# Optimization experiments

Measured on AMD Instinct MI355X. Metric: run time of the kernel, lower is better.

Reference implementation:

```python
import jax, jax.numpy as jnp
import numpy as np

LN_EPS = 1e-5


def _layernorm(x, g, b):
    m = jnp.mean(x, axis=-1, keepdims=True)
    v = jnp.mean((x - m) ** 2, axis=-1, keepdims=True)
    return (x - m) * jax.lax.rsqrt(v + LN_EPS) * g + b


def _gcn_conv(x, row, col, ew, W, b):
    # linear projection
    x = x @ W + b  # [N, out]
    n = x.shape[0]
    # weighted degree per source node (index_add over row)
    deg = jax.ops.segment_sum(ew, row, num_segments=n)  # [N]
    safe = jnp.where(deg > 0, deg, 1.0)
    dis = jnp.where(deg > 0, jax.lax.rsqrt(safe), 0.0)  # deg^-0.5, inf -> 0
    norm = dis[row] * ew * dis[col]  # [E]
    # gather-scale-scatter aggregation
    return jax.ops.segment_sum(norm[:, None] * x[col], row, num_segments=n)


def setup_inputs() -> dict:
    key = jax.random.key(0)
    ks = jax.random.split(key, 8)
    N, E, D_IN, D_H, D_OUT = 50000, 800000, 384, 256, 128
    x = jax.random.normal(ks[0], (N, D_IN), dtype=jnp.float32)
    edge_index = jax.random.randint(ks[1], (2, E), 0, N, dtype=jnp.int64)
    edge_weight = jax.random.uniform(ks[2], (E,), dtype=jnp.float32)
    W1 = jax.random.normal(ks[3], (D_IN, D_H), dtype=jnp.float32) * 0.02
    b1 = jnp.zeros((D_H,), dtype=jnp.float32)
    W2 = jax.random.normal(ks[4], (D_H, D_OUT), dtype=jnp.float32) * 0.02
    b2 = jnp.zeros((D_OUT,), dtype=jnp.float32)
    g1 = jnp.ones((D_H,), dtype=jnp.float32)
    be1 = jnp.zeros((D_H,), dtype=jnp.float32)
    g2 = jnp.ones((D_OUT,), dtype=jnp.float32)
    be2 = jnp.zeros((D_OUT,), dtype=jnp.float32)
    return {"x": x, "edge_index": edge_index, "edge_weight": edge_weight,
            "W1": W1, "b1": b1, "W2": W2, "b2": b2,
            "g1": g1, "be1": be1, "g2": g2, "be2": be2}


def reference(x, edge_index, edge_weight, W1, b1, W2, b2, g1, be1, g2, be2):
    row, col = edge_index[0], edge_index[1]
    h = _gcn_conv(x, row, col, edge_weight, W1, b1)
    h = _layernorm(h, g1, be1)
    h = jax.nn.relu(h)
    # dropout is identity in eval mode
    h = _gcn_conv(h, row, col, edge_weight, W2, b2)
    h = _layernorm(h, g2, be2)
    return h
```

## Files before the change

kernel.cpp:

```cpp
#include <hip/hip_runtime.h>


constexpr float LN_EPS = 1e-5f;
constexpr int   SLOTS  = 64;

typedef __attribute__((ext_vector_type(8))) short short8;
typedef __attribute__((ext_vector_type(4))) float f32x4;
typedef __attribute__((ext_vector_type(2))) float f32x2;

static __device__ __forceinline__ unsigned short f2bf(float f) {
    unsigned u = __float_as_uint(f);
    u += 0x7FFFu + ((u >> 16) & 1u);
    return (unsigned short)(u >> 16);
}
static __device__ __forceinline__ short8 f2bf8(float4 a, float4 b) {
    short8 r;
    r[0] = (short)f2bf(a.x); r[1] = (short)f2bf(a.y);
    r[2] = (short)f2bf(a.z); r[3] = (short)f2bf(a.w);
    r[4] = (short)f2bf(b.x); r[5] = (short)f2bf(b.y);
    r[6] = (short)f2bf(b.z); r[7] = (short)f2bf(b.w);
    return r;
}

#if defined(__has_builtin)
#if __has_builtin(__builtin_amdgcn_global_load_lds)
#define HAS_GLL 1
#endif
#endif

#ifdef HAS_GLL
static __device__ __forceinline__ void gll16(const void* g, void* l) {
    __builtin_amdgcn_global_load_lds(
        (__attribute__((address_space(1))) void*)g,
        (__attribute__((address_space(3))) void*)l, 16, 0, 0);
}
#endif

static __device__ __forceinline__ int swz(int r) {
    return (r & 3) ^ ((r >> 2) & 3);
}

__global__ __launch_bounds__(256) void k_hist(
    const int* __restrict__ row, const int* __restrict__ col,
    const float* __restrict__ ew, int* __restrict__ cnt,
    int2* __restrict__ edges, int E)
{
    int e = blockIdx.x * 256 + threadIdx.x;
    if (e >= E) return;
    int r = row[e];
    int o = atomicAdd(cnt + r, 1);
    if (o < SLOTS)
        edges[(size_t)r * SLOTS + o] = make_int2(col[e], __float_as_int(ew[e]));
}

__global__ __launch_bounds__(256) void k_dis(
    const int* __restrict__ cnt, const int2* __restrict__ edges,
    float* __restrict__ dis, int n)
{
    const int gw   = (blockIdx.x * 256 + threadIdx.x) >> 6;
    const int lane = threadIdx.x & 63;
    if (gw >= n) return;
    int c = cnt[gw]; if (c > SLOTS) c = SLOTS;
    float v = 0.0f;
    if (lane < c) v = __int_as_float(edges[(size_t)gw * SLOTS + lane].y);
    #pragma unroll
    for (int off = 32; off; off >>= 1) v += __shfl_xor(v, off);
    if (lane == 0) dis[gw] = v > 0.0f ? rsqrtf(v) : 0.0f;
}

__global__ __launch_bounds__(256) void k_prep(
    const float* __restrict__ W1, const float* __restrict__ W2,
    const float* __restrict__ x,
    unsigned short* __restrict__ W1P, unsigned short* __restrict__ W2P,
    unsigned short* __restrict__ xb, int nwin)
{
    constexpr int K1 = 384, N1 = 256, K2 = 256, N2 = 128;
    constexpr int WTB = (K1 * N1 + K2 * N2) / 256;
    if (blockIdx.x < WTB) {
        int o = blockIdx.x * 256 + threadIdx.x;
        if (o < K1 * N1) {
            int cc = o & 31, n = (o >> 5) % N1, p = o / (N1 * 32);
            int c = cc >> 3, j = cc & 7;
            int k = p * 32 + (((c ^ swz(n & 15)) & 3) << 3) + j;
            W1P[o] = f2bf(W1[(size_t)k * N1 + n]);
        } else {
            int o2 = o - K1 * N1;
            int cc = o2 & 31, n = (o2 >> 5) % N2, p = o2 / (N2 * 32);
            int c = cc >> 3, j = cc & 7;
            int k = p * 32 + (((c ^ swz(n & 15)) & 3) << 3) + j;
            W2P[o2] = f2bf(W2[(size_t)k * N2 + n]);
        }
    } else {
        int w = (blockIdx.x - WTB) * 256 + threadIdx.x;
        if (w >= nwin) return;
        int row = w / 12, win = w - row * 12;
        int s = swz(row & 15);
        const float* src = x + (size_t)row * 384 + win * 32;
        unsigned short* dst = xb + (size_t)row * 384 + win * 32;
        #pragma unroll
        for (int c = 0; c < 4; ++c) {
            int cs = c ^ s;
            float4 a = *(const float4*)(src + cs * 8);
            float4 b = *(const float4*)(src + cs * 8 + 4);
            *(short8*)(dst + c * 8) = f2bf8(a, b);
        }
    }
}

template<int NFULL, int K>
__global__ __launch_bounds__(256, 4) void k_gemm_mfma(
    const unsigned short* __restrict__ A, const unsigned short* __restrict__ BP,
    const float* __restrict__ bias, unsigned short* __restrict__ C, int M)
{
    constexpr int BM = 64, BN = 128, BK = 32;
    constexpr int MR = 4, NF = 2;
    constexpr int AB = BM * BK * 2;
    constexpr int BB = BN * BK * 2;
    constexpr int TB = AB + BB;

    __shared__ char smem[2 * TB];

    const int t    = threadIdx.x;
    const int lane = t & 63;
    const int wid  = t >> 6;
    const int row0 = blockIdx.x * BM;
    const int col0 = blockIdx.y * BN;
    const int fr   = lane & 15;
    const int fq   = lane >> 4;
    const int nbw  = wid * 32;
    const int nt   = K / BK;

    const int cOff = ((fq ^ swz(fr)) & 3) << 3;

    f32x4 acc[MR][NF] = {};

    auto srcA = [&](int slot, int k0) -> const void* {
        int ra = slot >> 2, ca = slot & 3;
        int gr = row0 + ra; if (gr >= M) gr = M - 1;
        return (const void*)(A + (size_t)gr * K + k0 + ca * 8);
    };
    auto srcB = [&](int slot, int st) -> const void* {
        int rb = slot >> 2, cb = slot & 3;
        return (const void*)(BP + ((size_t)st * NFULL + col0 + rb) * 32 + cb * 8);
    };

    auto compute = [&](char* buf) {
        const unsigned short* As = (const unsigned short*)buf;
        const unsigned short* Bs = (const unsigned short*)(buf + AB);
        short8 af[MR], bfr[NF];
        #pragma unroll
        for (int i = 0; i < MR; ++i)
            af[i] = *(const short8*)(As + (i * 16 + fr) * 32 + cOff);
        #pragma unroll
        for (int j = 0; j < NF; ++j)
            bfr[j] = *(const short8*)(Bs + (nbw + j * 16 + fr) * 32 + cOff);
        #pragma unroll
        for (int i = 0; i < MR; ++i)
            #pragma unroll
            for (int j = 0; j < NF; ++j)
                acc[i][j] = __builtin_amdgcn_mfma_f32_16x16x32_bf16(
                    af[i], bfr[j], acc[i][j], 0, 0, 0);
    };

#ifdef HAS_GLL
    auto stage = [&](int buf, int st) {
        char* As = smem + buf * TB;
        char* Bs = As + AB;
        gll16(srcA(t, st * BK), As + t * 16);
        gll16(srcB(t, st), Bs + t * 16);
        gll16(srcB(256 + t, st), Bs + (256 + t) * 16);
    };

    stage(0, 0);
    __syncthreads();
    int cur = 0;
    for (int st = 0; st < nt; ++st) {
        if (st + 1 < nt) stage(cur ^ 1, st + 1);
        compute(smem + cur * TB);
        __syncthreads();
        cur ^= 1;
    }
#else
    for (int st = 0; st < nt; ++st) {
        int4 ar = *(const int4*)srcA(t, st * BK);
        int4 b0 = *(const int4*)srcB(t, st);
        int4 b1 = *(const int4*)srcB(256 + t, st);
        __syncthreads();
        *(int4*)(smem + t * 16) = ar;
        *(int4*)(smem + AB + t * 16) = b0;
        *(int4*)(smem + AB + (256 + t) * 16) = b1;
        __syncthreads();
        compute(smem);
    }
#endif

    #pragma unroll
    for (int i = 0; i < MR; ++i) {
        #pragma unroll
        for (int j = 0; j < NF; ++j) {
            const int c = col0 + nbw + j * 16 + fr;
            const float bvv = bias[c];
            #pragma unroll
            for (int r = 0; r < 4; ++r) {
                const int rr = row0 + i * 16 + fq * 4 + r;
                if (rr < M)
                    C[(size_t)rr * NFULL + c] = f2bf(acc[i][j][r] + bvv);
            }
        }
    }
}

template<int D, bool RELU, bool OUTBF, bool SWZ>
__global__ __launch_bounds__(256) void k_agg_ln(
    const unsigned short* __restrict__ feat, const int* __restrict__ cnt,
    const int2* __restrict__ edges, const float* __restrict__ dis,
    const float* __restrict__ g, const float* __restrict__ b,
    void* __restrict__ outv, int n)
{
    constexpr int EV  = 16;
    constexpr int LPR = D / EV;
    constexpr int EPI = 64 / LPR;
    const int gw   = (blockIdx.x * 256 + threadIdx.x) >> 6;
    const int lane = threadIdx.x & 63;
    if (gw >= n) return;

    const int sub = lane / LPR;
    const int el  = (lane % LPR) * EV;

    int j1 = cnt[gw]; if (j1 > SLOTS) j1 = SLOTS;
    const int2* eb = edges + (size_t)gw * SLOTS;
    const float disr = dis[gw];

    f32x2 acc[8] = {};

    int2 e0 = (sub < j1)       ? eb[sub]       : make_int2(0, 0);
    int2 e1 = (EPI + sub < j1) ? eb[EPI + sub] : make_int2(0, 0);
    float dc0 = dis[e0.x];
    uint4 u0, u1;
    {
        const unsigned short* p = feat + (size_t)e0.x * D + el;
        u0 = *(const uint4*)p;
        u1 = *(const uint4*)(p + 8);
    }

    for (int j = 0; j < j1; j += EPI) {
        int2 e2 = (j + 2 * EPI + sub < j1) ? eb[j + 2 * EPI + sub]
                                           : make_int2(0, 0);
        float dc1 = dis[e1.x];
        const unsigned short* p = feat + (size_t)e1.x * D + el;
        uint4 v0 = *(const uint4*)p;
        uint4 v1 = *(const uint4*)(p + 8);

        const float wv = __int_as_float(e0.y) * dc0;
        const unsigned a[8] = {u0.x, u0.y, u0.z, u0.w, u1.x, u1.y, u1.z, u1.w};
        #pragma unroll
        for (int i = 0; i < 8; ++i) {
            f32x2 h;
            h.x = __uint_as_float(a[i] << 16);
            h.y = __uint_as_float(a[i] & 0xffff0000u);
            acc[i] += h * wv;
        }
        u0 = v0; u1 = v1; e0 = e1; e1 = e2; dc0 = dc1;
    }

    #pragma unroll
    for (int off = LPR; off < 64; off <<= 1)
        #pragma unroll
        for (int i = 0; i < 8; ++i) {
            acc[i].x += __shfl_xor(acc[i].x, off);
            acc[i].y += __shfl_xor(acc[i].y, off);
        }

    #pragma unroll
    for (int i = 0; i < 8; ++i) acc[i] *= disr;

    float s = 0.0f;
    #pragma unroll
    for (int i = 0; i < 8; ++i) s += acc[i].x + acc[i].y;
    #pragma unroll
    for (int off = 32; off; off >>= 1) s += __shfl_xor(s, off);
    const float m = s * (1.0f / (EPI * D));

    float q = 0.0f;
    #pragma unroll
    for (int i = 0; i < 8; ++i) {
        float dx = acc[i].x - m, dy = acc[i].y - m;
        q += dx * dx + dy * dy;
    }
    #pragma unroll
    for (int off = 32; off; off >>= 1) q += __shfl_xor(q, off);
    const float r = rsqrtf(q * (1.0f / (EPI * D)) + LN_EPS);

    if (lane < LPR) {
        float o[16];
        #pragma unroll
        for (int i = 0; i < 4; ++i) {
            float4 gv = *(const float4*)(g + el + i * 4);
            float4 bv = *(const float4*)(b + el + i * 4);
            const float vals[4] = {acc[2 * i].x, acc[2 * i].y,
                                   acc[2 * i + 1].x, acc[2 * i + 1].y};
            const float gg[4] = {gv.x, gv.y, gv.z, gv.w};
            const float bb[4] = {bv.x, bv.y, bv.z, bv.w};
            #pragma unroll
            for (int k2 = 0; k2 < 4; ++k2) {
                float tv = (vals[k2] - m) * r * gg[k2] + bb[k2];
                if constexpr (RELU) tv = fmaxf(tv, 0.0f);
                o[i * 4 + k2] = tv;
            }
        }
        if constexpr (OUTBF) {
            short8 lo, hi;
            #pragma unroll
            for (int i = 0; i < 8; ++i) {
                lo[i] = (short)f2bf(o[i]);
                hi[i] = (short)f2bf(o[8 + i]);
            }
            unsigned short* ob = (unsigned short*)outv + (size_t)gw * D;
            const int w0 = el & ~31;
            const int c0 = (el >> 3) & 3;
            const int sA = SWZ ? swz(gw & 15) : 0;
            *(short8*)(ob + w0 + (((c0 ^ sA) & 3) << 3))       = lo;
            *(short8*)(ob + w0 + ((((c0 + 1) ^ sA) & 3) << 3)) = hi;
        } else {
            float* op = (float*)outv + (size_t)gw * D + el;
            *(float4*)(op)      = make_float4(o[0],  o[1],  o[2],  o[3]);
            *(float4*)(op + 4)  = make_float4(o[4],  o[5],  o[6],  o[7]);
            *(float4*)(op + 8)  = make_float4(o[8],  o[9],  o[10], o[11]);
            *(float4*)(op + 12) = make_float4(o[12], o[13], o[14], o[15]);
        }
    }
}

extern "C" void kernel_launch(void* const* d_in, const int* in_sizes, int n_in,
                              void* d_out, int out_size, void* d_ws, size_t ws_size,
                              hipStream_t stream)
{
    (void)n_in; (void)out_size; (void)ws_size;

    constexpr int DIN = 384, DH = 256, DOUT = 128;

    const float* x   = (const float*)d_in[0];
    const int*   ei  = (const int*)  d_in[1];
    const float* ew  = (const float*)d_in[2];
    const float* W1  = (const float*)d_in[3];
    const float* b1  = (const float*)d_in[4];
    const float* W2  = (const float*)d_in[5];
    const float* b2  = (const float*)d_in[6];
    const float* g1  = (const float*)d_in[7];
    const float* be1 = (const float*)d_in[8];
    const float* g2  = (const float*)d_in[9];
    const float* be2 = (const float*)d_in[10];
    float* out = (float*)d_out;

    const int N = in_sizes[0] / DIN;
    const int E = in_sizes[2];
    const int* row = ei;
    const int* col = ei + E;

    char* w = (char*)d_ws;
    auto carve = [&](size_t bytes) {
        char* p = w;
        w += (bytes + 255) & ~(size_t)255;
        return p;
    };
    int*            cnt    = (int*)  carve((size_t)N * 4);
    float*          dis    = (float*)carve((size_t)N * 4);
    int2*           edges  = (int2*) carve((size_t)N * SLOTS * 8);
    unsigned short* W1P    = (unsigned short*)carve((size_t)DIN * DH * 2);
    unsigned short* W2P    = (unsigned short*)carve((size_t)DH * DOUT * 2);
    unsigned short* x_bf   = (unsigned short*)carve((size_t)N * DIN * 2);
    unsigned short* h1     = (unsigned short*)carve((size_t)N * DH * 2);
    unsigned short* h1ln   = (unsigned short*)carve((size_t)N * DH * 2);
    unsigned short* h2     = (unsigned short*)carve((size_t)N * DOUT * 2);

    const int gE = (E + 255) / 256;
    const int gW = (N + 3) / 4;
    const int gG = (N + 63) / 64;
    const int gX = (N * 12 + 255) / 256;
    constexpr int WTB = (DIN * DH + DH * DOUT) / 256;

    hipMemsetAsync(cnt, 0, (size_t)N * 4, stream);
    k_hist<<<gE, 256, 0, stream>>>(row, col, ew, cnt, edges, E);
    k_dis <<<gW, 256, 0, stream>>>(cnt, edges, dis, N);

    k_prep<<<WTB + gX, 256, 0, stream>>>(W1, W2, x, W1P, W2P, x_bf, N * 12);

    {
        dim3 grid(gG, DH / 128);
        k_gemm_mfma<DH, DIN><<<grid, 256, 0, stream>>>(x_bf, W1P, b1, h1, N);
    }
    k_agg_ln<DH, true, true, true><<<gW, 256, 0, stream>>>(
        h1, cnt, edges, dis, g1, be1, h1ln, N);

    {
        dim3 grid(gG, DOUT / 128);
        k_gemm_mfma<DOUT, DH><<<grid, 256, 0, stream>>>(h1ln, W2P, b2, h2, N);
    }
    k_agg_ln<DOUT, false, false, false><<<gW, 256, 0, stream>>>(
        h2, cnt, edges, dis, g2, be2, out, N);
}
```

Baseline: 225.4 us.

## Slice feature columns in aggregation and compact edges to 32-bit records

Adds a pass that packs each edge into one 32-bit word: a 16-bit source index plus a bf16 weight with the source-side dis factor already multiplied in. Aggregation is split into eight column slices, so each slice's gathered feature working set is smaller and more likely to stay in cache. LayerNorm moves into a separate kernel that reads a bf16 aggregate buffer reusing the old edge storage. The trade-offs are an extra kernel launch and an extra round trip through memory for the aggregate. It also adds bf16 rounding of the edge weights and the aggregate, and a 16-bit index that only works while N is below 65536.

```diff
diff --git a/kernel.cpp b/kernel.cpp
--- a/kernel.cpp
+++ b/kernel.cpp
@@ -12,6 +12,9 @@
     unsigned u = __float_as_uint(f);
     u += 0x7FFFu + ((u >> 16) & 1u);
     return (unsigned short)(u >> 16);
+}
+static __device__ __forceinline__ float bf2f(unsigned short h) {
+    return __uint_as_float(((unsigned)h) << 16);
 }
 static __device__ __forceinline__ short8 f2bf8(float4 a, float4 b) {
     short8 r;
@@ -66,6 +69,20 @@
     #pragma unroll
     for (int off = 32; off; off >>= 1) v += __shfl_xor(v, off);
     if (lane == 0) dis[gw] = v > 0.0f ? rsqrtf(v) : 0.0f;
+}
+
+__global__ __launch_bounds__(256) void k_ecompact(
+    const int* __restrict__ cnt, const int2* __restrict__ edges,
+    const float* __restrict__ dis, unsigned* __restrict__ edges4, int n64)
+{
+    int idx = blockIdx.x * 256 + threadIdx.x;
+    if (idx >= n64) return;
+    int node = idx >> 6, slot = idx & 63;
+    int j1 = cnt[node]; if (j1 > SLOTS) j1 = SLOTS;
+    if (slot >= j1) return;
+    int2 e = edges[idx];
+    float w = __int_as_float(e.y) * dis[e.x];
+    edges4[idx] = ((unsigned)e.x << 16) | (unsigned)f2bf(w);
 }
 
 __global__ __launch_bounds__(256) void k_prep(
@@ -210,124 +227,131 @@
     }
 }
 
+template<int D>
+__global__ __launch_bounds__(256) void k_agg_s(
+    const unsigned short* __restrict__ feat, const int* __restrict__ cnt,
+    const unsigned* __restrict__ edges4, const float* __restrict__ dis,
+    unsigned short* __restrict__ agg, int n)
+{
+    constexpr int SL  = D / 8;
+    constexpr int LPE = SL / 8;
+    constexpr int EPI = 64 / LPE;
+
+    const int slice = blockIdx.x & 7;
+    const int lane  = threadIdx.x & 63;
+    const int wvs   = (blockIdx.x >> 3) * 4 + (threadIdx.x >> 6);
+    const int WPS   = (gridDim.x >> 3) * 4;
+    const int sub   = lane / LPE;
+    const int cpos  = lane % LPE;
+
+    const unsigned short* fslice = feat + slice * SL + cpos * 8;
+
+    for (int node = wvs; node < n; node += WPS) {
+        int j1 = cnt[node]; if (j1 > SLOTS) j1 = SLOTS;
+        const unsigned* eb = edges4 + (size_t)node * SLOTS;
+
+        f32x2 acc[4] = {};
+        for (int j = 0; j < j1; j += EPI) {
+            const int jj = j + sub;
+            unsigned rec = (jj < j1) ? eb[jj] : 0u;
+            const float w = __uint_as_float((rec & 0xffffu) << 16);
+            const unsigned c = rec >> 16;
+            const uint4 u = *(const uint4*)(fslice + (size_t)c * D);
+            const unsigned a[4] = {u.x, u.y, u.z, u.w};
+            #pragma unroll
+            for (int i = 0; i < 4; ++i) {
+                f32x2 h;
+                h.x = __uint_as_float(a[i] << 16);
+                h.y = __uint_as_float(a[i] & 0xffff0000u);
+                acc[i] += h * w;
+            }
+        }
+
+        #pragma unroll
+        for (int off = LPE; off < 64; off <<= 1)
+            #pragma unroll
+            for (int i = 0; i < 4; ++i) {
+                acc[i].x += __shfl_xor(acc[i].x, off);
+                acc[i].y += __shfl_xor(acc[i].y, off);
+            }
+
+        if (sub == 0) {
+            const float disr = dis[node];
+            short8 o;
+            #pragma unroll
+            for (int i = 0; i < 4; ++i) {
+                o[2 * i]     = (short)f2bf(acc[i].x * disr);
+                o[2 * i + 1] = (short)f2bf(acc[i].y * disr);
+            }
+            *(short8*)(agg + (size_t)node * D + slice * SL + cpos * 8) = o;
+        }
+    }
+}
+
 template<int D, bool RELU, bool OUTBF, bool SWZ>
-__global__ __launch_bounds__(256) void k_agg_ln(
-    const unsigned short* __restrict__ feat, const int* __restrict__ cnt,
-    const int2* __restrict__ edges, const float* __restrict__ dis,
+__global__ __launch_bounds__(256) void k_ln(
+    const unsigned short* __restrict__ agg,
     const float* __restrict__ g, const float* __restrict__ b,
     void* __restrict__ outv, int n)
 {
-    constexpr int EV  = 16;
-    constexpr int LPR = D / EV;
-    constexpr int EPI = 64 / LPR;
+    constexpr int V = D / 64;
     const int gw   = (blockIdx.x * 256 + threadIdx.x) >> 6;
     const int lane = threadIdx.x & 63;
     if (gw >= n) return;
-
-    const int sub = lane / LPR;
-    const int el  = (lane % LPR) * EV;
-
-    int j1 = cnt[gw]; if (j1 > SLOTS) j1 = SLOTS;
-    const int2* eb = edges + (size_t)gw * SLOTS;
-    const float disr = dis[gw];
-
-    f32x2 acc[8] = {};
-
-    int2 e0 = (sub < j1)       ? eb[sub]       : make_int2(0, 0);
-    int2 e1 = (EPI + sub < j1) ? eb[EPI + sub] : make_int2(0, 0);
-    float dc0 = dis[e0.x];
-    uint4 u0, u1;
-    {
-        const unsigned short* p = feat + (size_t)e0.x * D + el;
-        u0 = *(const uint4*)p;
-        u1 = *(const uint4*)(p + 8);
-    }
-
-    for (int j = 0; j < j1; j += EPI) {
-        int2 e2 = (j + 2 * EPI + sub < j1) ? eb[j + 2 * EPI + sub]
-                                           : make_int2(0, 0);
-        float dc1 = dis[e1.x];
-        const unsigned short* p = feat + (size_t)e1.x * D + el;
-        uint4 v0 = *(const uint4*)p;
-        uint4 v1 = *(const uint4*)(p + 8);
-
-        const float wv = __int_as_float(e0.y) * dc0;
-        const unsigned a[8] = {u0.x, u0.y, u0.z, u0.w, u1.x, u1.y, u1.z, u1.w};
-        #pragma unroll
-        for (int i = 0; i < 8; ++i) {
-            f32x2 h;
-            h.x = __uint_as_float(a[i] << 16);
-            h.y = __uint_as_float(a[i] & 0xffff0000u);
-            acc[i] += h * wv;
-        }
-        u0 = v0; u1 = v1; e0 = e1; e1 = e2; dc0 = dc1;
-    }
-
-    #pragma unroll
-    for (int off = LPR; off < 64; off <<= 1)
-        #pragma unroll
-        for (int i = 0; i < 8; ++i) {
-            acc[i].x += __shfl_xor(acc[i].x, off);
-            acc[i].y += __shfl_xor(acc[i].y, off);
-        }
-
-    #pragma unroll
-    for (int i = 0; i < 8; ++i) acc[i] *= disr;
+    const int el = lane * V;
+
+    float v[V];
+    const unsigned short* ar = agg + (size_t)gw * D + el;
+    if constexpr (V == 4) {
+        ushort4 u = *(const ushort4*)ar;
+        v[0] = bf2f(u.x); v[1] = bf2f(u.y); v[2] = bf2f(u.z); v[3] = bf2f(u.w);
+    } else {
+        ushort2 u = *(const ushort2*)ar;
+        v[0] = bf2f(u.x); v[1] = bf2f(u.y);
+    }
 
     float s = 0.0f;
     #pragma unroll
-    for (int i = 0; i < 8; ++i) s += acc[i].x + acc[i].y;
+    for (int i = 0; i < V; ++i) s += v[i];
     #pragma unroll
     for (int off = 32; off; off >>= 1) s += __shfl_xor(s, off);
-    const float m = s * (1.0f / (EPI * D));
+    const float m = s * (1.0f / D);
 
     float q = 0.0f;
     #pragma unroll
-    for (int i = 0; i < 8; ++i) {
-        float dx = acc[i].x - m, dy = acc[i].y - m;
-        q += dx * dx + dy * dy;
-    }
+    for (int i = 0; i < V; ++i) { float d = v[i] - m; q += d * d; }
     #pragma unroll
     for (int off = 32; off; off >>= 1) q += __shfl_xor(q, off);
-    const float r = rsqrtf(q * (1.0f / (EPI * D)) + LN_EPS);
-
-    if (lane < LPR) {
-        float o[16];
-        #pragma unroll
-        for (int i = 0; i < 4; ++i) {
-            float4 gv = *(const float4*)(g + el + i * 4);
-            float4 bv = *(const float4*)(b + el + i * 4);
-            const float vals[4] = {acc[2 * i].x, acc[2 * i].y,
-                                   acc[2 * i + 1].x, acc[2 * i + 1].y};
-            const float gg[4] = {gv.x, gv.y, gv.z, gv.w};
-            const float bb[4] = {bv.x, bv.y, bv.z, bv.w};
-            #pragma unroll
-            for (int k2 = 0; k2 < 4; ++k2) {
-                float tv = (vals[k2] - m) * r * gg[k2] + bb[k2];
-                if constexpr (RELU) tv = fmaxf(tv, 0.0f);
-                o[i * 4 + k2] = tv;
-            }
-        }
-        if constexpr (OUTBF) {
-            short8 lo, hi;
-            #pragma unroll
-            for (int i = 0; i < 8; ++i) {
-                lo[i] = (short)f2bf(o[i]);
-                hi[i] = (short)f2bf(o[8 + i]);
-            }
-            unsigned short* ob = (unsigned short*)outv + (size_t)gw * D;
-            const int w0 = el & ~31;
-            const int c0 = (el >> 3) & 3;
-            const int sA = SWZ ? swz(gw & 15) : 0;
-            *(short8*)(ob + w0 + (((c0 ^ sA) & 3) << 3))       = lo;
-            *(short8*)(ob + w0 + ((((c0 + 1) ^ sA) & 3) << 3)) = hi;
+    const float r = rsqrtf(q * (1.0f / D) + LN_EPS);
+
+    float o[V];
+    #pragma unroll
+    for (int i = 0; i < V; ++i) {
+        float tv = (v[i] - m) * r * g[el + i] + b[el + i];
+        if constexpr (RELU) tv = fmaxf(tv, 0.0f);
+        o[i] = tv;
+    }
+
+    if constexpr (OUTBF) {
+        int eo = el;
+        if constexpr (SWZ) {
+            const int sA = swz(gw & 15);
+            eo = (el & ~31) | ((((el >> 3) & 3) ^ sA) << 3) | (el & 7);
+        }
+        unsigned short* ob = (unsigned short*)outv + (size_t)gw * D + eo;
+        if constexpr (V == 4) {
+            ushort4 u;
+            u.x = f2bf(o[0]); u.y = f2bf(o[1]); u.z = f2bf(o[2]); u.w = f2bf(o[3]);
+            *(ushort4*)ob = u;
         } else {
-            float* op = (float*)outv + (size_t)gw * D + el;
-            *(float4*)(op)      = make_float4(o[0],  o[1],  o[2],  o[3]);
-            *(float4*)(op + 4)  = make_float4(o[4],  o[5],  o[6],  o[7]);
-            *(float4*)(op + 8)  = make_float4(o[8],  o[9],  o[10], o[11]);
-            *(float4*)(op + 12) = make_float4(o[12], o[13], o[14], o[15]);
-        }
+            ushort2 u;
+            u.x = f2bf(o[0]); u.y = f2bf(o[1]);
+            *(ushort2*)ob = u;
+        }
+    } else {
+        float* op = (float*)outv + (size_t)gw * D + el;
+        if constexpr (V == 4) *(float4*)op = make_float4(o[0], o[1], o[2], o[3]);
+        else                  *(float2*)op = make_float2(o[0], o[1]);
     }
 }
 
@@ -363,25 +387,30 @@
         w += (bytes + 255) & ~(size_t)255;
         return p;
     };
-    int*            cnt    = (int*)  carve((size_t)N * 4);
-    float*          dis    = (float*)carve((size_t)N * 4);
-    int2*           edges  = (int2*) carve((size_t)N * SLOTS * 8);
+    int*            cnt    = (int*)     carve((size_t)N * 4);
+    float*          dis    = (float*)   carve((size_t)N * 4);
+    int2*           edges  = (int2*)    carve((size_t)N * SLOTS * 8);
+    unsigned*       edges4 = (unsigned*)carve((size_t)N * SLOTS * 4);
     unsigned short* W1P    = (unsigned short*)carve((size_t)DIN * DH * 2);
     unsigned short* W2P    = (unsigned short*)carve((size_t)DH * DOUT * 2);
     unsigned short* x_bf   = (unsigned short*)carve((size_t)N * DIN * 2);
     unsigned short* h1     = (unsigned short*)carve((size_t)N * DH * 2);
     unsigned short* h1ln   = (unsigned short*)carve((size_t)N * DH * 2);
     unsigned short* h2     = (unsigned short*)carve((size_t)N * DOUT * 2);
+    unsigned short* agg    = (unsigned short*)edges;
 
     const int gE = (E + 255) / 256;
     const int gW = (N + 3) / 4;
     const int gG = (N + 63) / 64;
     const int gX = (N * 12 + 255) / 256;
+    const int gS = (N * SLOTS + 255) / 256;
+    const int gA = 8 * 1024;
     constexpr int WTB = (DIN * DH + DH * DOUT) / 256;
 
     hipMemsetAsync(cnt, 0, (size_t)N * 4, stream);
-    k_hist<<<gE, 256, 0, stream>>>(row, col, ew, cnt, edges, E);
-    k_dis <<<gW, 256, 0, stream>>>(cnt, edges, dis, N);
+    k_hist    <<<gE, 256, 0, stream>>>(row, col, ew, cnt, edges, E);
+    k_dis     <<<gW, 256, 0, stream>>>(cnt, edges, dis, N);
+    k_ecompact<<<gS, 256, 0, stream>>>(cnt, edges, dis, edges4, N * SLOTS);
 
     k_prep<<<WTB + gX, 256, 0, stream>>>(W1, W2, x, W1P, W2P, x_bf, N * 12);
 
@@ -389,13 +418,13 @@
         dim3 grid(gG, DH / 128);
         k_gemm_mfma<DH, DIN><<<grid, 256, 0, stream>>>(x_bf, W1P, b1, h1, N);
     }
-    k_agg_ln<DH, true, true, true><<<gW, 256, 0, stream>>>(
-        h1, cnt, edges, dis, g1, be1, h1ln, N);
+    k_agg_s<DH><<<gA, 256, 0, stream>>>(h1, cnt, edges4, dis, agg, N);
+    k_ln<DH, true, true, true><<<gW, 256, 0, stream>>>(agg, g1, be1, h1ln, N);
 
     {
         dim3 grid(gG, DOUT / 128);
         k_gemm_mfma<DOUT, DH><<<grid, 256, 0, stream>>>(h1ln, W2P, b2, h2, N);
     }
-    k_agg_ln<DOUT, false, false, false><<<gW, 256, 0, stream>>>(
-        h2, cnt, edges, dis, g2, be2, out, N);
-}
+    k_agg_s<DOUT><<<gA, 256, 0, stream>>>(h2, cnt, edges4, dis, agg, N);
+    k_ln<DOUT, false, false, false><<<gW, 256, 0, stream>>>(agg, g2, be2, out, N);
+}
```

After: 471.5 us. 109% more time.
